# Kernel tuning notes

Measured on AMD Instinct MI355X. Metric: run time of the kernel, lower is better.

## Reference

```python
import jax, jax.numpy as jnp
import numpy as np

B, S, H = 2, 2048, 2048
NH, NKV, HD = 32, 8, 64          # num_heads, num_kv_heads, head_dim
G = NH // NKV                     # GQA group size
NEG = -1e9


def setup_inputs() -> dict:
    key = jax.random.key(0)
    ks = jax.random.split(key, 8)
    x = jax.random.normal(ks[0], (B, S, H), dtype=jnp.float32)
    # real RoPE frequencies: theta = 10000 ** (-2i/hd)
    inv_freq = 1.0 / (10000.0 ** (np.arange(0, HD, 2, dtype=np.float32) / HD))
    angles = np.arange(S, dtype=np.float32)[:, None] * inv_freq[None, :]  # [S, HD//2]
    freqs_cos = jnp.asarray(np.cos(angles))
    freqs_sin = jnp.asarray(np.sin(angles))
    # additive causal mask [S, S]
    mask = jnp.where(jnp.tril(jnp.ones((S, S), dtype=bool)), 0.0, NEG).astype(jnp.float32)
    sc = 0.02
    Wq = jax.random.normal(ks[1], (NH * HD, H), dtype=jnp.float32) * sc
    bq = jax.random.normal(ks[2], (NH * HD,), dtype=jnp.float32) * sc
    Wk = jax.random.normal(ks[3], (NKV * HD, H), dtype=jnp.float32) * sc
    bk = jax.random.normal(ks[4], (NKV * HD,), dtype=jnp.float32) * sc
    Wv = jax.random.normal(ks[5], (NKV * HD, H), dtype=jnp.float32) * sc
    bv = jax.random.normal(ks[6], (NKV * HD,), dtype=jnp.float32) * sc
    Wo = jax.random.normal(ks[7], (H, NH * HD), dtype=jnp.float32) * sc
    return {"x": x, "freqs_cos": freqs_cos, "freqs_sin": freqs_sin, "mask": mask,
            "Wq": Wq, "bq": bq, "Wk": Wk, "bk": bk, "Wv": Wv, "bv": bv, "Wo": Wo}


def _rotate_half(t):
    h = t.shape[-1] // 2
    return jnp.concatenate([-t[..., h:], t[..., :h]], axis=-1)


def reference(x, freqs_cos, freqs_sin, mask, Wq, bq, Wk, bk, Wv, bv, Wo):
    b, s, _ = x.shape
    q = (x @ Wq.T + bq).reshape(b, s, NH, HD)
    k = (x @ Wk.T + bk).reshape(b, s, NKV, HD)
    v = (x @ Wv.T + bv).reshape(b, s, NKV, HD)
    # RoPE (rotate_half style): cos/sin duplicated along last dim -> [1, s, 1, HD]
    cos = jnp.concatenate([freqs_cos, freqs_cos], axis=-1)[None, :, None, :]
    sin = jnp.concatenate([freqs_sin, freqs_sin], axis=-1)[None, :, None, :]
    q = q * cos + _rotate_half(q) * sin
    k = k * cos + _rotate_half(k) * sin
    # GQA: view q as [b, s, NKV, G, HD]; avoids repeat_interleave of K/V (same math)
    q5 = q.reshape(b, s, NKV, G, HD)
    scores = jnp.einsum('bqhgd,bkhd->bhgqk', q5, k) / jnp.sqrt(jnp.float32(HD))
    scores = scores + mask  # broadcast [s, s] over [b, h, g, s, s]
    p = jax.nn.softmax(scores.astype(jnp.float32), axis=-1).astype(q.dtype)
    out = jnp.einsum('bhgqk,bkhd->bqhgd', p, v).reshape(b, s, NH * HD)
    return out @ Wo.T
```

## Files before the change

### kernel.cpp

```cpp
#include <hip/hip_runtime.h>
#include <hip/hip_bf16.h>
#include <cstddef>
#include <cstdint>

#define B_   2
#define S_   2048
#define H_   2048
#define NH_  32
#define NKV_ 8
#define HD_  64

typedef __attribute__((ext_vector_type(8))) short short8;
typedef __attribute__((ext_vector_type(4))) float v4f;
typedef __attribute__((ext_vector_type(16))) float v16f;

#define MAXC 48.0f
#define QSCALE 0.18033688011112042f

__device__ __forceinline__ unsigned short f2b(float f) {
    unsigned int u = __float_as_uint(f);
    u += 0x7FFFu + ((u >> 16) & 1u);
    return (unsigned short)(u >> 16);
}
__device__ __forceinline__ unsigned int pkbf(float a, float b) {
    __hip_bfloat162 h = __float22bfloat162_rn(float2{a, b});
    return *(unsigned int*)&h;
}
__device__ __forceinline__ v4f mfma16(short8 a, short8 b, v4f c) {
    return __builtin_amdgcn_mfma_f32_16x16x32_bf16(a, b, c, 0, 0, 0);
}
__device__ __forceinline__ v16f mfma32(short8 a, short8 b, v16f c) {
    return __builtin_amdgcn_mfma_f32_32x32x16_bf16(a, b, c, 0, 0, 0);
}
__device__ __forceinline__ void gll16(void* lds, const void* g) {
    __builtin_amdgcn_global_load_lds(
        (const __attribute__((address_space(1))) unsigned int*)g,
        (__attribute__((address_space(3))) unsigned int*)lds, 16, 0, 0);
}

__global__ __launch_bounds__(256) void convert_all(
    const float* __restrict__ x, const float* __restrict__ wq,
    const float* __restrict__ wk, const float* __restrict__ wv,
    const float* __restrict__ wo,
    unsigned short* __restrict__ xb, unsigned short* __restrict__ wqb,
    unsigned short* __restrict__ wkb, unsigned short* __restrict__ wvb,
    unsigned short* __restrict__ wob)
{
    size_t i = ((size_t)blockIdx.x * 256 + threadIdx.x) * 4;
    const float* src; unsigned short* dst; size_t off;
    if (i < 8388608)       { src = x;  dst = xb;  off = i; }
    else if (i < 12582912) { src = wq; dst = wqb; off = i - 8388608; }
    else if (i < 13631488) { src = wk; dst = wkb; off = i - 12582912; }
    else if (i < 14680064) { src = wv; dst = wvb; off = i - 13631488; }
    else                   { src = wo; dst = wob; off = i - 14680064; }
    float4 v = *(const float4*)(src + off);
    ushort4 o;
    o.x = f2b(v.x); o.y = f2b(v.y); o.z = f2b(v.z); o.w = f2b(v.w);
    *(ushort4*)(dst + off) = o;
}

__global__ __launch_bounds__(256) void qkv_gemm(
    const unsigned short* __restrict__ xb,
    const unsigned short* __restrict__ wqb, const unsigned short* __restrict__ wkb,
    const unsigned short* __restrict__ wvb,
    const float* __restrict__ bq, const float* __restrict__ bk,
    const float* __restrict__ bv,
    const float* __restrict__ fc, const float* __restrict__ fs,
    unsigned short* __restrict__ Qb, unsigned short* __restrict__ Kb,
    unsigned short* __restrict__ Vt)
{
    __shared__ unsigned short As[128 * 64];
    __shared__ unsigned short Bs[128 * 64];
    const int tid = threadIdx.x;
    const int lane = tid & 63, w = tid >> 6;
    const int tx = lane & 15, quad = lane >> 4;
    const int bx = blockIdx.x, by = blockIdx.y;

    const unsigned short *Ap, *Bp;
    int mode, aBase, bBase;
    if (bx < 16)      { mode = 0; Ap = xb;  Bp = wqb; aBase = by * 128; bBase = bx * 128; }
    else if (bx < 20) { mode = 1; Ap = xb;  Bp = wkb; aBase = by * 128; bBase = (bx - 16) * 128; }
    else              { mode = 2; Ap = wvb; Bp = xb;  aBase = (bx - 20) * 128; bBase = by * 128; }

    const int wm = (w >> 1) * 64, wn = (w & 1) * 64;
    v4f acc[4][4];
#pragma unroll
    for (int i = 0; i < 4; ++i)
#pragma unroll
        for (int j = 0; j < 4; ++j) acc[i][j] = (v4f)0.f;

    const int r8 = lane >> 3, gc = (lane & 7) ^ r8;
    const unsigned short* ga = &Ap[(size_t)(aBase + w * 32 + r8) * 2048 + gc * 8];
    const unsigned short* gb = &Bp[(size_t)(bBase + w * 32 + r8) * 2048 + gc * 8];

    const int t7 = tx & 7;
    int slA[2], slB[2];
#pragma unroll
    for (int kk = 0; kk < 2; ++kk) { slA[kk] = ((kk * 4 + quad) ^ t7) * 8; slB[kk] = slA[kk]; }

    for (int k0 = 0; k0 < 2048; k0 += 64) {
        __syncthreads();
#pragma unroll
        for (int i = 0; i < 4; ++i) {
            gll16(&As[(w * 32 + i * 8) * 64], ga + (size_t)(i * 8) * 2048 + k0);
            gll16(&Bs[(w * 32 + i * 8) * 64], gb + (size_t)(i * 8) * 2048 + k0);
        }
        __syncthreads();
#pragma unroll
        for (int kk = 0; kk < 2; ++kk) {
            short8 af[4], bf[4];
#pragma unroll
            for (int mt = 0; mt < 4; ++mt)
                af[mt] = *(const short8*)&As[(wm + mt * 16 + tx) * 64 + slA[kk]];
#pragma unroll
            for (int nt = 0; nt < 4; ++nt)
                bf[nt] = *(const short8*)&Bs[(wn + nt * 16 + tx) * 64 + slB[kk]];
#pragma unroll
            for (int mt = 0; mt < 4; ++mt)
#pragma unroll
                for (int nt = 0; nt < 4; ++nt)
                    acc[mt][nt] = mfma16(af[mt], bf[nt], acc[mt][nt]);
        }
    }

    if (mode <= 1) {
        unsigned short* Cout = mode ? Kb : Qb;
        const float* bias    = mode ? bk : bq;
        const int ldN        = mode ? 512 : 2048;
        const float scq      = mode ? 1.0f : QSCALE;
        float bx0 = bias[bBase + wn +  0 + tx];
        float bx1 = bias[bBase + wn + 16 + tx];
        float bx2 = bias[bBase + wn + 32 + tx];
        float bx3 = bias[bBase + wn + 48 + tx];
#pragma unroll
        for (int mt = 0; mt < 4; ++mt)
#pragma unroll
            for (int rg = 0; rg < 4; ++rg) {
                int m = aBase + wm + mt * 16 + quad * 4 + rg;
                int s = m & (S_ - 1);
                float c0 = fc[s * 32 + tx],      c1 = fc[s * 32 + 16 + tx];
                float s0 = fs[s * 32 + tx],      s1 = fs[s * 32 + 16 + tx];
                float q0 = acc[mt][0][rg] + bx0, q1 = acc[mt][1][rg] + bx1;
                float q2 = acc[mt][2][rg] + bx2, q3 = acc[mt][3][rg] + bx3;
                size_t base = (size_t)m * ldN + bBase + wn + tx;
                Cout[base]      = f2b((q0 * c0 - q2 * s0) * scq);
                Cout[base + 16] = f2b((q1 * c1 - q3 * s1) * scq);
                Cout[base + 32] = f2b((q2 * c0 + q0 * s0) * scq);
                Cout[base + 48] = f2b((q3 * c1 + q1 * s1) * scq);
            }
    } else {
#pragma unroll
        for (int mt = 0; mt < 4; ++mt)
#pragma unroll
            for (int rg = 0; rg < 4; ++rg) {
                int d = aBase + wm + mt * 16 + quad * 4 + rg;
                float bvv = bv[d];
                size_t base = (size_t)d * 4096 + bBase + wn + tx;
#pragma unroll
                for (int nt = 0; nt < 4; ++nt)
                    Vt[base + nt * 16] = f2b(acc[mt][nt][rg] + bvv);
            }
    }
}

__global__ __launch_bounds__(256) void out_gemm(
    const unsigned short* __restrict__ Ab, const unsigned short* __restrict__ Bw,
    float* __restrict__ C)
{
    __shared__ unsigned short As[128 * 64];
    __shared__ unsigned short Bs[128 * 64];
    const int tid = threadIdx.x;
    const int lane = tid & 63, w = tid >> 6;
    const int tx = lane & 15, quad = lane >> 4;
    const int bm = blockIdx.y * 128, bn = blockIdx.x * 128;
    const int wm = (w >> 1) * 64, wn = (w & 1) * 64;

    v4f acc[4][4];
#pragma unroll
    for (int i = 0; i < 4; ++i)
#pragma unroll
        for (int j = 0; j < 4; ++j) acc[i][j] = (v4f)0.f;

    const int r8 = lane >> 3, gc = (lane & 7) ^ r8;
    const unsigned short* ga = &Ab[(size_t)(bm + w * 32 + r8) * 2048 + gc * 8];
    const unsigned short* gb = &Bw[(size_t)(bn + w * 32 + r8) * 2048 + gc * 8];
    const int t7 = tx & 7;
    int sl[2];
#pragma unroll
    for (int kk = 0; kk < 2; ++kk) sl[kk] = ((kk * 4 + quad) ^ t7) * 8;

    for (int k0 = 0; k0 < 2048; k0 += 64) {
        __syncthreads();
#pragma unroll
        for (int i = 0; i < 4; ++i) {
            gll16(&As[(w * 32 + i * 8) * 64], ga + (size_t)(i * 8) * 2048 + k0);
            gll16(&Bs[(w * 32 + i * 8) * 64], gb + (size_t)(i * 8) * 2048 + k0);
        }
        __syncthreads();
#pragma unroll
        for (int kk = 0; kk < 2; ++kk) {
            short8 af[4], bf[4];
#pragma unroll
            for (int mt = 0; mt < 4; ++mt)
                af[mt] = *(const short8*)&As[(wm + mt * 16 + tx) * 64 + sl[kk]];
#pragma unroll
            for (int nt = 0; nt < 4; ++nt)
                bf[nt] = *(const short8*)&Bs[(wn + nt * 16 + tx) * 64 + sl[kk]];
#pragma unroll
            for (int mt = 0; mt < 4; ++mt)
#pragma unroll
                for (int nt = 0; nt < 4; ++nt)
                    acc[mt][nt] = mfma16(af[mt], bf[nt], acc[mt][nt]);
        }
    }
#pragma unroll
    for (int mt = 0; mt < 4; ++mt)
#pragma unroll
        for (int nt = 0; nt < 4; ++nt)
#pragma unroll
            for (int rg = 0; rg < 4; ++rg) {
                int m = bm + wm + mt * 16 + quad * 4 + rg;
                C[(size_t)m * 2048 + bn + wn + nt * 16 + tx] = acc[mt][nt][rg];
            }
}

__global__ __launch_bounds__(256) void attn_mfma(
    const unsigned short* __restrict__ Q, const unsigned short* __restrict__ K,
    const unsigned short* __restrict__ Vt, unsigned short* __restrict__ O)
{
    __shared__ __align__(16) unsigned short smem[2 * 64 * 72];
    unsigned short* Ks = smem;
    unsigned short* Vs = smem + 64 * 72;
    const int tid = threadIdx.x;
    const int lane = tid & 63, wq = tid >> 6;
    const int l32 = lane & 31, half = lane >> 5;
    const int qh = wq & 1;
    const int ts = wq >> 1;
    const int p = blockIdx.x;
    const int h = blockIdx.y, b = blockIdx.z;
    const int kvh = h >> 2;

    const int srow = tid >> 3, sc8 = (tid & 7) * 8;

    for (int ph = 0; ph < 2; ++ph) {
        const int T = ph ? (31 - p) : p;

        const int qrow = T * 64 + qh * 32 + l32;
        const unsigned short* Qr = &Q[(((size_t)b * S_ + qrow) * NH_ + h) * HD_];
        short8 qf[4];
#pragma unroll
        for (int s = 0; s < 4; ++s)
            qf[s] = *(const short8*)(Qr + s * 16 + half * 8);

        float la = 0.f, lb = 0.f, lc = 0.f, ld = 0.f;
        v16f o0 = (v16f)0.f, o1 = (v16f)0.f;

        for (int kt = 0; kt <= T; ++kt) {
            __syncthreads();
#pragma unroll
            for (int i = 0; i < 2; ++i) {
                int row = srow + i * 32;
                *(uint4*)&Ks[row * 72 + sc8] =
                    *(const uint4*)&K[(((size_t)b * S_ + kt * 64 + row) * NKV_ + kvh) * HD_ + sc8];
                *(uint4*)&Vs[row * 72 + sc8] =
                    *(const uint4*)&Vt[(size_t)(kvh * 64 + row) * 4096 + b * 2048 + kt * 64 + sc8];
            }
            __syncthreads();
            const bool diag = (kt == T);
            if (diag && ts > qh) continue;
            const bool part = diag && (ts == qh);

            const int kb = (ts * 32 + l32) * 72 + half * 8;
            v16f st = (v16f)(-MAXC);
            __builtin_amdgcn_s_setprio(1);
            st = mfma32(*(const short8*)&Ks[kb],      qf[0], st);
            st = mfma32(*(const short8*)&Ks[kb + 16], qf[1], st);
            st = mfma32(*(const short8*)&Ks[kb + 32], qf[2], st);
            st = mfma32(*(const short8*)&Ks[kb + 48], qf[3], st);
            __builtin_amdgcn_s_setprio(0);

            float pv[16];
#pragma unroll
            for (int r = 0; r < 16; ++r) pv[r] = exp2f(st[r]);
            if (part) {
#pragma unroll
                for (int r = 0; r < 16; ++r) {
                    int krow = (r & 3) + 8 * (r >> 2) + 4 * half;
                    if (krow > l32) pv[r] = 0.f;
                }
            }
            la += (pv[0]  + pv[1])  + (pv[2]  + pv[3]);
            lb += (pv[4]  + pv[5])  + (pv[6]  + pv[7]);
            lc += (pv[8]  + pv[9])  + (pv[10] + pv[11]);
            ld += (pv[12] + pv[13]) + (pv[14] + pv[15]);

            unsigned int u[8];
#pragma unroll
            for (int g = 0; g < 4; ++g) {
                u[2 * g]     = pkbf(pv[4 * g],     pv[4 * g + 1]);
                u[2 * g + 1] = pkbf(pv[4 * g + 2], pv[4 * g + 3]);
            }
#pragma unroll
            for (int sg = 0; sg < 2; ++sg) {
                unsigned int a0 = u[4 * sg], a1 = u[4 * sg + 1];
                unsigned int b0 = u[4 * sg + 2], b1 = u[4 * sg + 3];
                uint4 fw;
#if __has_builtin(__builtin_amdgcn_permlane32_swap)
                typedef unsigned int u2v __attribute__((ext_vector_type(2)));
                u2v r0 = __builtin_amdgcn_permlane32_swap(a0, b0, false, false);
                u2v r1 = __builtin_amdgcn_permlane32_swap(a1, b1, false, false);
                fw.x = r0[0]; fw.y = r1[0]; fw.z = r0[1]; fw.w = r1[1];
#else
                unsigned int s0 = __shfl_xor((int)a0, 32);
                unsigned int s1 = __shfl_xor((int)a1, 32);
                unsigned int s2 = __shfl_xor((int)b0, 32);
                unsigned int s3 = __shfl_xor((int)b1, 32);
                fw.x = half ? s2 : a0;
                fw.y = half ? s3 : a1;
                fw.z = half ? b0 : s0;
                fw.w = half ? b1 : s1;
#endif
                short8 pf = *(short8*)&fw;
                const int vo = (2 * ts + sg) * 16 + half * 8;
                __builtin_amdgcn_s_setprio(1);
                o0 = mfma32(*(const short8*)&Vs[l32 * 72 + vo],        pf, o0);
                o1 = mfma32(*(const short8*)&Vs[(32 + l32) * 72 + vo], pf, o1);
                __builtin_amdgcn_s_setprio(0);
            }
        }

        float l = (la + lb) + (lc + ld);
        l += __shfl_xor(l, 32);

        __syncthreads();
        float* red = (float*)smem;
        const int rbase = (qh * 64 + lane) * 33;
        if (ts == 1) {
#pragma unroll
            for (int r = 0; r < 16; ++r) { red[rbase + r] = o0[r]; red[rbase + 16 + r] = o1[r]; }
            red[rbase + 32] = l;
        }
        __syncthreads();
        if (ts == 0) {
#pragma unroll
            for (int r = 0; r < 16; ++r) { o0[r] += red[rbase + r]; o1[r] += red[rbase + 16 + r]; }
            l += red[rbase + 32];
            float inv = 1.f / l;
            int qg = T * 64 + qh * 32 + l32;
            unsigned short* orow = &O[((size_t)b * S_ + qg) * (NH_ * HD_) + h * HD_];
#pragma unroll
            for (int td = 0; td < 2; ++td) {
                const v16f& oo = td ? o1 : o0;
#pragma unroll
                for (int g = 0; g < 4; ++g) {
                    int d = td * 32 + g * 8 + half * 4;
                    uint2 uu;
                    uu.x = pkbf(oo[4 * g] * inv,     oo[4 * g + 1] * inv);
                    uu.y = pkbf(oo[4 * g + 2] * inv, oo[4 * g + 3] * inv);
                    *(uint2*)&orow[d] = uu;
                }
            }
        }
    }
}

extern "C" void kernel_launch(void* const* d_in, const int* in_sizes, int n_in,
                              void* d_out, int out_size, void* d_ws, size_t ws_size,
                              hipStream_t stream)
{
    const float* x  = (const float*)d_in[0];
    const float* fc = (const float*)d_in[1];
    const float* fs = (const float*)d_in[2];
    const float* Wq = (const float*)d_in[4];
    const float* bq = (const float*)d_in[5];
    const float* Wk = (const float*)d_in[6];
    const float* bk = (const float*)d_in[7];
    const float* Wv = (const float*)d_in[8];
    const float* bv = (const float*)d_in[9];
    const float* Wo = (const float*)d_in[10];
    float* out = (float*)d_out;

    unsigned short* ws = (unsigned short*)d_ws;
    unsigned short* xb  = ws;
    unsigned short* wqb = ws + 8388608;
    unsigned short* wkb = ws + 12582912;
    unsigned short* wvb = ws + 13631488;
    unsigned short* wob = ws + 14680064;
    unsigned short* Qb  = ws + 18874368;
    unsigned short* Kb  = ws + 27262976;
    unsigned short* Vt  = ws + 29360128;
    unsigned short* Ob  = ws + 31457280;

    dim3 blk(256);
    convert_all<<<18432, blk, 0, stream>>>(x, Wq, Wk, Wv, Wo, xb, wqb, wkb, wvb, wob);
    qkv_gemm<<<dim3(24, 32), blk, 0, stream>>>(xb, wqb, wkb, wvb, bq, bk, bv,
                                               fc, fs, Qb, Kb, Vt);
    attn_mfma<<<dim3(16, NH_, B_), blk, 0, stream>>>(Qb, Kb, Vt, Ob);
    out_gemm<<<dim3(16, 32), blk, 0, stream>>>(Ob, wob, out);
}
```

Baseline: 334.4 us.

## Double-buffer attention K/V tiles with direct global-to-LDS loads and XOR swizzle

Replaces the register-staged K/V tile copy in the attention kernel with direct global-to-LDS loads (gll16) into two alternating buffers, so the next tile is prefetched while the current one is consumed. The padded 72-stride LDS layout becomes an unpadded 64-stride layout with an XOR column swizzle to avoid bank conflicts. One barrier per iteration replaces two. The cost is doubled LDS use, which may lower occupancy, and an explicit vmcnt(0) wait plus an extra barrier between phases.

```diff
diff --git a/kernel.cpp b/kernel.cpp
--- a/kernel.cpp
+++ b/kernel.cpp
@@ -228,9 +228,7 @@
     const unsigned short* __restrict__ Q, const unsigned short* __restrict__ K,
     const unsigned short* __restrict__ Vt, unsigned short* __restrict__ O)
 {
-    __shared__ __align__(16) unsigned short smem[2 * 64 * 72];
-    unsigned short* Ks = smem;
-    unsigned short* Vs = smem + 64 * 72;
+    __shared__ __align__(16) unsigned short smem[16384];
     const int tid = threadIdx.x;
     const int lane = tid & 63, wq = tid >> 6;
     const int l32 = lane & 31, half = lane >> 5;
@@ -240,7 +238,18 @@
     const int h = blockIdx.y, b = blockIdx.z;
     const int kvh = h >> 2;
 
-    const int srow = tid >> 3, sc8 = (tid & 7) * 8;
+    const int r8 = lane >> 3, gc7 = (lane & 7) ^ r8;
+    const unsigned short* gk0 = &K[(((size_t)b * S_ + wq * 16 + r8) * NKV_ + kvh) * HD_ + gc7 * 8];
+    const unsigned short* gv0 = &Vt[(size_t)(kvh * 64 + wq * 16 + r8) * 4096 + (size_t)b * 2048 + gc7 * 8];
+    unsigned short* KdBase = smem + wq * 16 * 64;
+    unsigned short* VdBase = smem + 4096 + wq * 16 * 64;
+
+    const int r7 = l32 & 7;
+    int skk[4], svo[2];
+#pragma unroll
+    for (int kk = 0; kk < 4; ++kk) skk[kk] = (((kk * 2 + half) ^ r7)) * 8;
+#pragma unroll
+    for (int sg = 0; sg < 2; ++sg) svo[sg] = ((((2 * ts + sg) * 2 + half) ^ r7)) * 8;
 
     for (int ph = 0; ph < 2; ++ph) {
         const int T = ph ? (31 - p) : p;
@@ -255,28 +264,43 @@
         float la = 0.f, lb = 0.f, lc = 0.f, ld = 0.f;
         v16f o0 = (v16f)0.f, o1 = (v16f)0.f;
 
+        {
+            const unsigned short* gk = gk0;
+            const unsigned short* gv = gv0;
+            gll16(KdBase,       gk);
+            gll16(KdBase + 512, gk + 8 * 512);
+            gll16(VdBase,       gv);
+            gll16(VdBase + 512, gv + (size_t)8 * 4096);
+        }
+        int cur = 0;
+
         for (int kt = 0; kt <= T; ++kt) {
+            asm volatile("s_waitcnt vmcnt(0)" ::: "memory");
             __syncthreads();
-#pragma unroll
-            for (int i = 0; i < 2; ++i) {
-                int row = srow + i * 32;
-                *(uint4*)&Ks[row * 72 + sc8] =
-                    *(const uint4*)&K[(((size_t)b * S_ + kt * 64 + row) * NKV_ + kvh) * HD_ + sc8];
-                *(uint4*)&Vs[row * 72 + sc8] =
-                    *(const uint4*)&Vt[(size_t)(kvh * 64 + row) * 4096 + b * 2048 + kt * 64 + sc8];
-            }
-            __syncthreads();
+            if (kt < T) {
+                const int nb = (cur ^ 1) * 8192;
+                const unsigned short* gk = gk0 + (size_t)(kt + 1) * 64 * 512;
+                const unsigned short* gv = gv0 + (kt + 1) * 64;
+                gll16(KdBase + nb,       gk);
+                gll16(KdBase + nb + 512, gk + 8 * 512);
+                gll16(VdBase + nb,       gv);
+                gll16(VdBase + nb + 512, gv + (size_t)8 * 4096);
+            }
+            const unsigned short* Ksb = smem + cur * 8192;
+            const unsigned short* Vsb = Ksb + 4096;
+            cur ^= 1;
+
             const bool diag = (kt == T);
             if (diag && ts > qh) continue;
             const bool part = diag && (ts == qh);
 
-            const int kb = (ts * 32 + l32) * 72 + half * 8;
+            const int kbase = (ts * 32 + l32) * 64;
             v16f st = (v16f)(-MAXC);
             __builtin_amdgcn_s_setprio(1);
-            st = mfma32(*(const short8*)&Ks[kb],      qf[0], st);
-            st = mfma32(*(const short8*)&Ks[kb + 16], qf[1], st);
-            st = mfma32(*(const short8*)&Ks[kb + 32], qf[2], st);
-            st = mfma32(*(const short8*)&Ks[kb + 48], qf[3], st);
+            st = mfma32(*(const short8*)&Ksb[kbase + skk[0]], qf[0], st);
+            st = mfma32(*(const short8*)&Ksb[kbase + skk[1]], qf[1], st);
+            st = mfma32(*(const short8*)&Ksb[kbase + skk[2]], qf[2], st);
+            st = mfma32(*(const short8*)&Ksb[kbase + skk[3]], qf[3], st);
             __builtin_amdgcn_s_setprio(0);
 
             float pv[16];
@@ -321,10 +345,9 @@
                 fw.w = half ? b1 : s1;
 #endif
                 short8 pf = *(short8*)&fw;
-                const int vo = (2 * ts + sg) * 16 + half * 8;
                 __builtin_amdgcn_s_setprio(1);
-                o0 = mfma32(*(const short8*)&Vs[l32 * 72 + vo],        pf, o0);
-                o1 = mfma32(*(const short8*)&Vs[(32 + l32) * 72 + vo], pf, o1);
+                o0 = mfma32(*(const short8*)&Vsb[l32 * 64 + svo[sg]],        pf, o0);
+                o1 = mfma32(*(const short8*)&Vsb[(32 + l32) * 64 + svo[sg]], pf, o1);
                 __builtin_amdgcn_s_setprio(0);
             }
         }
@@ -361,6 +384,7 @@
                 }
             }
         }
+        if (ph == 0) __syncthreads();
     }
 }
 
```

Result: faster. 323.4 us (-3.3%).

## Double-buffer K/V tiles with register prefetch in attention kernel

Applied to the files above, without the earlier changes.

The attention loop now prefetches the next K/V tile into registers while computing on the current one, then writes it into an alternating LDS buffer, so each iteration needs one barrier instead of two. The exp2 call is swapped for the raw hardware exp2 builtin, and launch bounds now request 4 blocks per CU. This aims to hide global-load latency behind the MFMA work. In exchange it doubles LDS use, adds register pressure from the prefetch, and adds an extra barrier between phases to keep the shared reduction buffer safe.

```diff
diff --git a/kernel.cpp b/kernel.cpp
--- a/kernel.cpp
+++ b/kernel.cpp
@@ -25,6 +25,13 @@
 __device__ __forceinline__ unsigned int pkbf(float a, float b) {
     __hip_bfloat162 h = __float22bfloat162_rn(float2{a, b});
     return *(unsigned int*)&h;
+}
+__device__ __forceinline__ float fexp2(float x) {
+#if __has_builtin(__builtin_amdgcn_exp2f)
+    return __builtin_amdgcn_exp2f(x);
+#else
+    return exp2f(x);
+#endif
 }
 __device__ __forceinline__ v4f mfma16(short8 a, short8 b, v4f c) {
     return __builtin_amdgcn_mfma_f32_16x16x32_bf16(a, b, c, 0, 0, 0);
@@ -224,13 +231,11 @@
             }
 }
 
-__global__ __launch_bounds__(256) void attn_mfma(
+__global__ __launch_bounds__(256, 4) void attn_mfma(
     const unsigned short* __restrict__ Q, const unsigned short* __restrict__ K,
     const unsigned short* __restrict__ Vt, unsigned short* __restrict__ O)
 {
-    __shared__ __align__(16) unsigned short smem[2 * 64 * 72];
-    unsigned short* Ks = smem;
-    unsigned short* Vs = smem + 64 * 72;
+    __shared__ __align__(16) unsigned short smem[2][2][64 * 72];
     const int tid = threadIdx.x;
     const int lane = tid & 63, wq = tid >> 6;
     const int l32 = lane & 31, half = lane >> 5;
@@ -241,6 +246,9 @@
     const int kvh = h >> 2;
 
     const int srow = tid >> 3, sc8 = (tid & 7) * 8;
+    const unsigned short* gkB = &K[(((size_t)b * S_ + srow) * NKV_ + kvh) * HD_ + sc8];
+    const unsigned short* gvB = &Vt[(size_t)(kvh * 64 + srow) * 4096 + (size_t)b * 2048 + sc8];
+    const int woff = srow * 72 + sc8;
 
     for (int ph = 0; ph < 2; ++ph) {
         const int T = ph ? (31 - p) : p;
@@ -255,17 +263,32 @@
         float la = 0.f, lb = 0.f, lc = 0.f, ld = 0.f;
         v16f o0 = (v16f)0.f, o1 = (v16f)0.f;
 
+        uint4 kr0 = *(const uint4*)(gkB);
+        uint4 kr1 = *(const uint4*)(gkB + 32 * (NKV_ * HD_));
+        uint4 vr0 = *(const uint4*)(gvB);
+        uint4 vr1 = *(const uint4*)(gvB + (size_t)32 * 4096);
+        int cur = 0;
+
         for (int kt = 0; kt <= T; ++kt) {
+            unsigned short* Kw = &smem[cur][0][woff];
+            unsigned short* Vw = &smem[cur][1][woff];
+            *(uint4*)(Kw)           = kr0;
+            *(uint4*)(Kw + 32 * 72) = kr1;
+            *(uint4*)(Vw)           = vr0;
+            *(uint4*)(Vw + 32 * 72) = vr1;
             __syncthreads();
-#pragma unroll
-            for (int i = 0; i < 2; ++i) {
-                int row = srow + i * 32;
-                *(uint4*)&Ks[row * 72 + sc8] =
-                    *(const uint4*)&K[(((size_t)b * S_ + kt * 64 + row) * NKV_ + kvh) * HD_ + sc8];
-                *(uint4*)&Vs[row * 72 + sc8] =
-                    *(const uint4*)&Vt[(size_t)(kvh * 64 + row) * 4096 + b * 2048 + kt * 64 + sc8];
-            }
-            __syncthreads();
+            if (kt < T) {
+                const unsigned short* gk = gkB + (size_t)(kt + 1) * 64 * (NKV_ * HD_);
+                const unsigned short* gv = gvB + (kt + 1) * 64;
+                kr0 = *(const uint4*)(gk);
+                kr1 = *(const uint4*)(gk + 32 * (NKV_ * HD_));
+                vr0 = *(const uint4*)(gv);
+                vr1 = *(const uint4*)(gv + (size_t)32 * 4096);
+            }
+            const unsigned short* Ksb = smem[cur][0];
+            const unsigned short* Vsb = smem[cur][1];
+            cur ^= 1;
+
             const bool diag = (kt == T);
             if (diag && ts > qh) continue;
             const bool part = diag && (ts == qh);
@@ -273,15 +296,15 @@
             const int kb = (ts * 32 + l32) * 72 + half * 8;
             v16f st = (v16f)(-MAXC);
             __builtin_amdgcn_s_setprio(1);
-            st = mfma32(*(const short8*)&Ks[kb],      qf[0], st);
-            st = mfma32(*(const short8*)&Ks[kb + 16], qf[1], st);
-            st = mfma32(*(const short8*)&Ks[kb + 32], qf[2], st);
-            st = mfma32(*(const short8*)&Ks[kb + 48], qf[3], st);
+            st = mfma32(*(const short8*)&Ksb[kb],      qf[0], st);
+            st = mfma32(*(const short8*)&Ksb[kb + 16], qf[1], st);
+            st = mfma32(*(const short8*)&Ksb[kb + 32], qf[2], st);
+            st = mfma32(*(const short8*)&Ksb[kb + 48], qf[3], st);
             __builtin_amdgcn_s_setprio(0);
 
             float pv[16];
 #pragma unroll
-            for (int r = 0; r < 16; ++r) pv[r] = exp2f(st[r]);
+            for (int r = 0; r < 16; ++r) pv[r] = fexp2(st[r]);
             if (part) {
 #pragma unroll
                 for (int r = 0; r < 16; ++r) {
@@ -323,8 +346,8 @@
                 short8 pf = *(short8*)&fw;
                 const int vo = (2 * ts + sg) * 16 + half * 8;
                 __builtin_amdgcn_s_setprio(1);
-                o0 = mfma32(*(const short8*)&Vs[l32 * 72 + vo],        pf, o0);
-                o1 = mfma32(*(const short8*)&Vs[(32 + l32) * 72 + vo], pf, o1);
+                o0 = mfma32(*(const short8*)&Vsb[l32 * 72 + vo],        pf, o0);
+                o1 = mfma32(*(const short8*)&Vsb[(32 + l32) * 72 + vo], pf, o1);
                 __builtin_amdgcn_s_setprio(0);
             }
         }
@@ -333,7 +356,7 @@
         l += __shfl_xor(l, 32);
 
         __syncthreads();
-        float* red = (float*)smem;
+        float* red = (float*)&smem[0][0][0];
         const int rbase = (qh * 64 + lane) * 33;
         if (ts == 1) {
 #pragma unroll
@@ -361,6 +384,7 @@
                 }
             }
         }
+        if (ph == 0) __syncthreads();
     }
 }
 
```

Result: faster. 312.7 us (-6.5%).
